# Kernel tuning notes

Hardware: AMD Instinct MI355X
Metric: run time of the kernel (lower is better)

Reference implementation:

```python
import jax, jax.numpy as jnp
import numpy as np

B, H, W, C = 64, 28, 28, 384
G = 7
N = G * G                  # tokens per window = 49
NH, HD = 12, 32            # heads, head_dim
SCALE = HD ** -0.5
EPS = 1e-5


def _make_bias_coords():
    # biases: all relative (dh, dw) offsets, shape [(2G-1)^2, 2]
    r = np.arange(1 - G, G)
    biases = np.stack(np.meshgrid(r, r, indexing='ij')).reshape(2, -1).T.astype(np.float32)
    # relative_position_index: [N, N] lookup into the bias table
    coords = np.stack(np.meshgrid(np.arange(G), np.arange(G), indexing='ij')).reshape(2, -1)
    rel = coords[:, :, None] - coords[:, None, :]          # [2, N, N]
    rel = rel.transpose(1, 2, 0)                            # [N, N, 2]
    rel[:, :, 0] += G - 1
    rel[:, :, 1] += G - 1
    rel[:, :, 0] *= 2 * G - 1
    idx = rel.sum(-1)                                       # [N, N]
    return jnp.asarray(biases), jnp.asarray(idx, dtype=jnp.int32)

BIASES, REL_IDX = _make_bias_coords()


def _ln(x, g, b):
    m = jnp.mean(x, -1, keepdims=True)
    v = jnp.var(x, -1, keepdims=True)
    return (x - m) * jax.lax.rsqrt(v + EPS) * g + b


def _pos_bias(ppw, ppb, l1g, l1b, p1w, p1b, l2g, l2b, p2w, p2b, l3g, l3b, p3w, p3b):
    # DynamicPosBias with residual=False: pos3(pos2(pos1(pos_proj(biases))))
    pos = BIASES @ ppw + ppb                                # [169, 24]
    pos = jax.nn.relu(_ln(pos, l1g, l1b)) @ p1w + p1b
    pos = jax.nn.relu(_ln(pos, l2g, l2b)) @ p2w + p2b
    pos = jax.nn.relu(_ln(pos, l3g, l3b)) @ p3w + p3b       # [169, NH]
    # gather -> [N, N, NH] -> [NH, N, N]
    return pos[REL_IDX.reshape(-1)].reshape(N, N, NH).transpose(2, 0, 1)


def _forward(x, norm1_g, norm1_b, qkv_w, qkv_b, proj_w, proj_b,
             norm2_g, norm2_b, fc1_w, fc1_b, fc2_w, fc2_b,
             pp_w, pp_b, l1_g, l1_b, p1_w, p1_b, l2_g, l2_b, p2_w, p2_b,
             l3_g, l3_b, p3_w, p3_b):
    shortcut = x
    h = _ln(x, norm1_g, norm1_b).reshape(B, H, W, C)
    # SDA (lsda_flag=0) window partition: [B, H/G, G, W/G, G, C] -> windows
    h = h.reshape(B, H // G, G, W // G, G, C).transpose(0, 1, 3, 2, 4, 5)
    h = h.reshape(-1, N, C)                                 # [B*nW, N, C]
    Bw = h.shape[0]

    qkv = (h @ qkv_w + qkv_b).reshape(Bw, N, 3, NH, HD).transpose(2, 0, 3, 1, 4)
    q, k, v = qkv[0] * SCALE, qkv[1], qkv[2]                # [Bw, NH, N, HD]

    bias = _pos_bias(pp_w, pp_b, l1_g, l1_b, p1_w, p1_b,
                     l2_g, l2_b, p2_w, p2_b, l3_g, l3_b, p3_w, p3_b)
    attn = jnp.einsum('bhnd,bhmd->bhnm', q, k) + bias[None]  # [Bw, NH, N, N]
    attn = jax.nn.softmax(attn, axis=-1)

    o = jnp.einsum('bhnm,bhmd->bhnd', attn, v)
    o = o.transpose(0, 2, 1, 3).reshape(Bw, N, C)
    o = o @ proj_w + proj_b

    # reverse window partition
    o = o.reshape(B, H // G, W // G, G, G, C).transpose(0, 1, 3, 2, 4, 5)
    o = o.reshape(B, H * W, C)

    x = shortcut + o
    y = _ln(x, norm2_g, norm2_b)
    y = jax.nn.gelu(y @ fc1_w + fc1_b, approximate=False) @ fc2_w + fc2_b
    return x + y


def setup_inputs() -> dict:
    key = jax.random.key(0)
    ks = iter(jax.random.split(key, 32))
    s = 0.02
    PD = 24  # pos_dim = (dim // 4) // 4
    MH = 4 * C

    def rn(k, shape):
        return jax.random.normal(k, shape, dtype=jnp.float32) * s

    return {
        'x': jax.random.normal(next(ks), (B, H * W, C), dtype=jnp.float32),
        'norm1_g': jnp.ones((C,), jnp.float32), 'norm1_b': jnp.zeros((C,), jnp.float32),
        'qkv_w': rn(next(ks), (C, 3 * C)), 'qkv_b': jnp.zeros((3 * C,), jnp.float32),
        'proj_w': rn(next(ks), (C, C)), 'proj_b': jnp.zeros((C,), jnp.float32),
        'norm2_g': jnp.ones((C,), jnp.float32), 'norm2_b': jnp.zeros((C,), jnp.float32),
        'fc1_w': rn(next(ks), (C, MH)), 'fc1_b': jnp.zeros((MH,), jnp.float32),
        'fc2_w': rn(next(ks), (MH, C)), 'fc2_b': jnp.zeros((C,), jnp.float32),
        'pp_w': rn(next(ks), (2, PD)), 'pp_b': jnp.zeros((PD,), jnp.float32),
        'l1_g': jnp.ones((PD,), jnp.float32), 'l1_b': jnp.zeros((PD,), jnp.float32),
        'p1_w': rn(next(ks), (PD, PD)), 'p1_b': jnp.zeros((PD,), jnp.float32),
        'l2_g': jnp.ones((PD,), jnp.float32), 'l2_b': jnp.zeros((PD,), jnp.float32),
        'p2_w': rn(next(ks), (PD, PD)), 'p2_b': jnp.zeros((PD,), jnp.float32),
        'l3_g': jnp.ones((PD,), jnp.float32), 'l3_b': jnp.zeros((PD,), jnp.float32),
        'p3_w': rn(next(ks), (PD, NH)), 'p3_b': jnp.zeros((NH,), jnp.float32),
    }


def reference(x, norm1_g, norm1_b, qkv_w, qkv_b, proj_w, proj_b,
              norm2_g, norm2_b, fc1_w, fc1_b, fc2_w, fc2_b,
              pp_w, pp_b, l1_g, l1_b, p1_w, p1_b, l2_g, l2_b, p2_w, p2_b,
              l3_g, l3_b, p3_w, p3_b):
    return _forward(x, norm1_g, norm1_b, qkv_w, qkv_b, proj_w, proj_b,
                    norm2_g, norm2_b, fc1_w, fc1_b, fc2_w, fc2_b,
                    pp_w, pp_b, l1_g, l1_b, p1_w, p1_b, l2_g, l2_b, p2_w, p2_b,
                    l3_g, l3_b, p3_w, p3_b)
```

## Files before the change

### kernel.cpp

```cpp
#include <hip/hip_runtime.h>

typedef unsigned short u16;
typedef short s16x8 __attribute__((ext_vector_type(8)));
typedef short s16x4 __attribute__((ext_vector_type(4)));
typedef float f32x4 __attribute__((ext_vector_type(4)));
typedef float f32x2 __attribute__((ext_vector_type(2)));

#define B_ 64
#define Hh 28
#define Ww 28
#define Cc 384
#define Gg 7
#define Nn 49
#define NH 12
#define HD 32
#define TT 50176
#define NWIN 1024
#define QKV_ELEMS 19267584u
#define SCALE_Q 0.17677669529663687f

__device__ __forceinline__ float b2f(u16 u) {
  union { unsigned int i; float f; } v; v.i = ((unsigned int)u) << 16; return v.f;
}
__device__ __forceinline__ u16 f2b(float f) {
  union { float f; unsigned int i; } v; v.f = f;
  unsigned int r = v.i + 0x7fffu + ((v.i >> 16) & 1u);
  return (u16)(r >> 16);
}

__device__ __forceinline__ void gload_lds16(const u16* g, u16* l) {
  __builtin_amdgcn_global_load_lds(
      (const __attribute__((address_space(1))) unsigned int*)(const void*)g,
      (__attribute__((address_space(3))) unsigned int*)(void*)l, 16, 0, 0);
}

__global__ void transpose_all(const float* __restrict__ w0, u16* __restrict__ o0,
                              const float* __restrict__ w1, u16* __restrict__ o1,
                              const float* __restrict__ w2, u16* __restrict__ o2,
                              const float* __restrict__ w3, u16* __restrict__ o3) {
  int b = blockIdx.x;
  const float* in; u16* out; int K, N, base;
  if (b < 1728)      { in = w0; out = o0; K = 384;  N = 1152; base = b; }
  else if (b < 2304) { in = w1; out = o1; K = 384;  N = 384;  base = b - 1728; }
  else if (b < 4608) { in = w2; out = o2; K = 384;  N = 1536; base = b - 2304; }
  else               { in = w3; out = o3; K = 1536; N = 384;  base = b - 4608; }
  int i = base * 256 + threadIdx.x;
  if (i < K * N) {
    int k = i / N, n = i % N;
    out[(size_t)n * K + k] = f2b(in[i]);
  }
}

__global__ __launch_bounds__(256)
void pos_mlp_kernel(const float* __restrict__ pp_w, const float* __restrict__ pp_b,
                    const float* __restrict__ l1g, const float* __restrict__ l1b,
                    const float* __restrict__ p1w, const float* __restrict__ p1b,
                    const float* __restrict__ l2g, const float* __restrict__ l2b,
                    const float* __restrict__ p2w, const float* __restrict__ p2b,
                    const float* __restrict__ l3g, const float* __restrict__ l3b,
                    const float* __restrict__ p3w, const float* __restrict__ p3b,
                    float* __restrict__ pos169) {
  __shared__ float w0[48], bb0[24], g1[24], e1[24], w1[576], bb1[24],
                   g2[24], e2[24], w2[576], bb2[24], g3[24], e3[24], w3[288], bb3[12];
  int tid = threadIdx.x;
  for (int i = tid; i < 48; i += 256) w0[i] = pp_w[i];
  for (int i = tid; i < 24; i += 256) {
    bb0[i] = pp_b[i]; g1[i] = l1g[i]; e1[i] = l1b[i]; bb1[i] = p1b[i];
    g2[i] = l2g[i]; e2[i] = l2b[i]; bb2[i] = p2b[i];
    g3[i] = l3g[i]; e3[i] = l3b[i];
  }
  for (int i = tid; i < 576; i += 256) { w1[i] = p1w[i]; w2[i] = p2w[i]; }
  for (int i = tid; i < 288; i += 256) w3[i] = p3w[i];
  for (int i = tid; i < 12; i += 256) bb3[i] = p3b[i];
  __syncthreads();
  if (tid < 169) {
    float bi = (float)(tid / 13) - 6.f, bj = (float)(tid % 13) - 6.f;
    float cur[24], t[24];
    #pragma unroll
    for (int c = 0; c < 24; c++) cur[c] = bi * w0[c] + bj * w0[24 + c] + bb0[c];

    auto lnrelu = [&](const float* gg, const float* ee) {
      float s = 0.f, sq = 0.f;
      #pragma unroll
      for (int c = 0; c < 24; c++) { s += cur[c]; sq += cur[c] * cur[c]; }
      float mean = s * (1.f / 24.f);
      float var = sq * (1.f / 24.f) - mean * mean;
      float rstd = rsqrtf(var + 1e-5f);
      #pragma unroll
      for (int c = 0; c < 24; c++)
        t[c] = fmaxf(0.f, (cur[c] - mean) * rstd * gg[c] + ee[c]);
    };

    lnrelu(g1, e1);
    #pragma unroll
    for (int o = 0; o < 24; o++) {
      float a = bb1[o];
      #pragma unroll
      for (int c = 0; c < 24; c++) a += t[c] * w1[c * 24 + o];
      cur[o] = a;
    }
    lnrelu(g2, e2);
    #pragma unroll
    for (int o = 0; o < 24; o++) {
      float a = bb2[o];
      #pragma unroll
      for (int c = 0; c < 24; c++) a += t[c] * w2[c * 24 + o];
      cur[o] = a;
    }
    lnrelu(g3, e3);
    #pragma unroll
    for (int h = 0; h < 12; h++) {
      float a = bb3[h];
      #pragma unroll
      for (int c = 0; c < 24; c++) a += t[c] * w3[c * 12 + h];
      pos169[tid * 12 + h] = a;
    }
  }
}

__global__ __launch_bounds__(256)
void ln_kernel(const float* __restrict__ x, const float* __restrict__ g,
               const float* __restrict__ be, u16* __restrict__ out) {
  int wid = threadIdx.x >> 6, lane = threadIdx.x & 63;
  size_t row = (size_t)blockIdx.x * 4 + wid;
  const float* xr = x + row * Cc;
  float v[6];
  float s = 0.f, sq = 0.f;
  #pragma unroll
  for (int p = 0; p < 3; p++) {
    f32x2 u = *(const f32x2*)&xr[p * 128 + lane * 2];
    v[2 * p] = u.x; v[2 * p + 1] = u.y;
    s += u.x + u.y; sq += u.x * u.x + u.y * u.y;
  }
  #pragma unroll
  for (int off = 32; off > 0; off >>= 1) { s += __shfl_xor(s, off); sq += __shfl_xor(sq, off); }
  float mean = s * (1.f / 384.f);
  float var = sq * (1.f / 384.f) - mean * mean;
  float rstd = rsqrtf(var + 1e-5f);
  u16* orow = out + row * Cc;
  #pragma unroll
  for (int p = 0; p < 3; p++) {
    int c = p * 128 + lane * 2;
    f32x2 ug = *(const f32x2*)&g[c];
    f32x2 ub = *(const f32x2*)&be[c];
    float o0 = (v[2 * p] - mean) * rstd * ug.x + ub.x;
    float o1 = (v[2 * p + 1] - mean) * rstd * ug.y + ub.y;
    unsigned int uo = (unsigned int)f2b(o0) | ((unsigned int)f2b(o1) << 16);
    *(unsigned int*)&orow[c] = uo;
  }
}

template <int EPI>
__global__ __launch_bounds__(256, 4)
void gemm_k(const u16* __restrict__ A, const u16* __restrict__ Bt,
            const float* __restrict__ bias, const void* resv, void* outv,
            int K, int gridX, int rowoff) {
  __shared__ u16 As[2][4096];
  __shared__ u16 Bs[2][4096];
  const int tid = threadIdx.x;
  const int wid = tid >> 6, lane = tid & 63;
  const int wr = (wid >> 1) * 64, wc = (wid & 1) * 64;
  const int lm = lane & 15, lq = lane >> 4;

  const int total = gridDim.x;
  const int xcd = blockIdx.x & 7, pos = blockIdx.x >> 3;
  const int cbase = total >> 3, crem = total & 7;
  const int tile = (xcd < crem) ? (xcd * (cbase + 1) + pos)
                                : (crem * (cbase + 1) + (xcd - crem) * cbase + pos);
  const int mTile = tile / gridX;
  const int nTile = tile - mTile * gridX;
  const int mBase = mTile * 128, nBase = nTile * 128;

  const int srow = tid >> 2;
  const int sg = (tid & 3) ^ ((tid >> 3) & 3);
  const size_t aRow0 = (size_t)(mBase + srow) * K + sg * 8;
  const size_t aRow1 = (size_t)(mBase + 64 + srow) * K + sg * 8;
  const size_t bRow0 = (size_t)(nBase + srow) * K + sg * 8;
  const size_t bRow1 = (size_t)(nBase + 64 + srow) * K + sg * 8;

  int aslot[4], bslot[4];
  #pragma unroll
  for (int i = 0; i < 4; i++) {
    int ar = wr + i * 16 + lm;
    aslot[i] = ar * 32 + (lq ^ ((ar >> 1) & 3)) * 8;
    int br = wc + i * 16 + lm;
    bslot[i] = br * 32 + (lq ^ ((br >> 1) & 3)) * 8;
  }

  auto stage = [&](int k0, int b) {
    gload_lds16(A + aRow0 + k0, As[b] + tid * 8);
    gload_lds16(A + aRow1 + k0, As[b] + 2048 + tid * 8);
    gload_lds16(Bt + bRow0 + k0, Bs[b] + tid * 8);
    gload_lds16(Bt + bRow1 + k0, Bs[b] + 2048 + tid * 8);
  };

  const int kIters = K >> 5;
  f32x4 acc[4][4] = {};
  stage(0, 0);
  __syncthreads();
  for (int k = 0; k < kIters; k++) {
    const int cb = k & 1;
    if (k + 1 < kIters) stage((k + 1) << 5, cb ^ 1);
    s16x8 af[4], bfr[4];
    #pragma unroll
    for (int i = 0; i < 4; i++) af[i] = *(const s16x8*)&As[cb][aslot[i]];
    #pragma unroll
    for (int j = 0; j < 4; j++) bfr[j] = *(const s16x8*)&Bs[cb][bslot[j]];
    #pragma unroll
    for (int i = 0; i < 4; i++)
      #pragma unroll
      for (int j = 0; j < 4; j++)
        acc[i][j] = __builtin_amdgcn_mfma_f32_16x16x32_bf16(af[i], bfr[j], acc[i][j], 0, 0, 0);
    __syncthreads();
  }

  int colA[4]; float bvv[4];
  #pragma unroll
  for (int j = 0; j < 4; j++) {
    colA[j] = nBase + wc + j * 16 + lm;
    bvv[j] = bias[colA[j]];
  }

  if constexpr (EPI == 0) {
    u16* out = (u16*)outv;
    size_t offj[4]; float scl[4];
    #pragma unroll
    for (int j = 0; j < 4; j++) {
      int col = colA[j];
      int qi = col / 384, c2 = col % 384;
      int head = c2 >> 5, d = c2 & 31;
      offj[j] = (size_t)qi * QKV_ELEMS + (size_t)head * 1568 + d;
      scl[j] = (qi == 0) ? SCALE_Q : 1.0f;
    }
    #pragma unroll
    for (int i = 0; i < 4; i++) {
      #pragma unroll
      for (int rg = 0; rg < 4; rg++) {
        int t = mBase + wr + i * 16 + lq * 4 + rg;
        int b_ = t / 784, rr = t % 784;
        int hh = rr / 28, ww = rr % 28;
        int widx = b_ * 16 + (hh / 7) * 4 + (ww / 7);
        int n = (hh % 7) * 7 + (ww % 7);
        size_t offr = (size_t)widx * 18816 + n * 32;
        #pragma unroll
        for (int j = 0; j < 4; j++)
          out[offj[j] + offr] = f2b((acc[i][j][rg] + bvv[j]) * scl[j]);
      }
    }
  } else if constexpr (EPI == 1) {
    float* out = (float*)outv;
    const float* res = (const float*)resv;
    #pragma unroll
    for (int i = 0; i < 4; i++) {
      #pragma unroll
      for (int rg = 0; rg < 4; rg++) {
        size_t rb = (size_t)(rowoff + mBase + wr + i * 16 + lq * 4 + rg) * 384;
        #pragma unroll
        for (int j = 0; j < 4; j++) {
          size_t o = rb + colA[j];
          out[o] = acc[i][j][rg] + bvv[j] + res[o];
        }
      }
    }
  } else {
    u16* out = (u16*)outv;
    #pragma unroll
    for (int i = 0; i < 4; i++) {
      #pragma unroll
      for (int rg = 0; rg < 4; rg++) {
        size_t rb = (size_t)(mBase + wr + i * 16 + lq * 4 + rg) * 1536;
        #pragma unroll
        for (int j = 0; j < 4; j++) {
          float v = acc[i][j][rg] + bvv[j];
          float gl = 0.5f * v * (1.0f + erff(v * 0.70710678118654752f));
          out[rb + colA[j]] = f2b(gl);
        }
      }
    }
  }
}

__global__ __launch_bounds__(256, 3)
void attn_mfma(const u16* __restrict__ qkv, const float* __restrict__ pos169,
               u16* __restrict__ attn_out) {
  __shared__ u16 P_l[4][64 * 68];
  __shared__ float bias_l[4][170];
  const int wid = threadIdx.x >> 6, lane = threadIdx.x & 63;
  const int lm = lane & 15, lq = lane >> 4;
  const int pair = blockIdx.x * 4 + wid;
  const int widx = pair / 12, head = pair % 12;
  const u16* qp = qkv + (size_t)widx * 18816 + head * 1568;
  const u16* kp = qp + QKV_ELEMS;
  const u16* vp = kp + QKV_ELEMS;

  for (int i = lane; i < 169; i += 64) bias_l[wid][i] = pos169[i * 12 + head];

  s16x8 aq[4], bk[4];
  #pragma unroll
  for (int i = 0; i < 4; i++) aq[i] = *(const s16x8*)&qp[(i * 16 + lm) * 32 + lq * 8];
  #pragma unroll
  for (int j = 0; j < 4; j++) bk[j] = *(const s16x8*)&kp[(j * 16 + lm) * 32 + lq * 8];

  f32x4 acc[4][4] = {};
  #pragma unroll
  for (int i = 0; i < 4; i++)
    #pragma unroll
    for (int j = 0; j < 4; j++)
      acc[i][j] = __builtin_amdgcn_mfma_f32_16x16x32_bf16(aq[i], bk[j], acc[i][j], 0, 0, 0);

  int mj[4], mhj[4], mwj[4];
  #pragma unroll
  for (int j = 0; j < 4; j++) {
    mj[j] = j * 16 + lm; mhj[j] = mj[j] / 7; mwj[j] = mj[j] - mhj[j] * 7;
  }

  #pragma unroll
  for (int i = 0; i < 4; i++) {
    #pragma unroll
    for (int rg = 0; rg < 4; rg++) {
      int n = i * 16 + lq * 4 + rg;
      int nh = n / 7, nw = n - nh * 7;
      float s[4];
      #pragma unroll
      for (int j = 0; j < 4; j++) {
        int idx = (nh - mhj[j] + 6) * 13 + (nw - mwj[j] + 6);
        idx = min(max(idx, 0), 168);
        s[j] = acc[i][j][rg] + bias_l[wid][idx];
        if (mj[j] >= 49) s[j] = -3.0e30f;
      }
      float mx = fmaxf(fmaxf(s[0], s[1]), fmaxf(s[2], s[3]));
      #pragma unroll
      for (int off = 1; off < 16; off <<= 1) mx = fmaxf(mx, __shfl_xor(mx, off));
      float e[4];
      float sm = 0.f;
      #pragma unroll
      for (int j = 0; j < 4; j++) { e[j] = __expf(s[j] - mx); sm += e[j]; }
      #pragma unroll
      for (int off = 1; off < 16; off <<= 1) sm += __shfl_xor(sm, off);
      float r = 1.0f / sm;
      #pragma unroll
      for (int j = 0; j < 4; j++)
        P_l[wid][n * 68 + mj[j]] = f2b(e[j] * r);
    }
  }

  s16x8 ap[4][2];
  #pragma unroll
  for (int i = 0; i < 4; i++)
    #pragma unroll
    for (int ks = 0; ks < 2; ks++) {
      const u16* p = &P_l[wid][(i * 16 + lm) * 68 + ks * 32 + lq * 8];
      s16x4 lo = *(const s16x4*)p;
      s16x4 hi = *(const s16x4*)(p + 4);
      ap[i][ks] = __builtin_shufflevector(lo, hi, 0, 1, 2, 3, 4, 5, 6, 7);
    }
  s16x8 bv[2][2];
  #pragma unroll
  for (int jt = 0; jt < 2; jt++)
    #pragma unroll
    for (int ks = 0; ks < 2; ks++) {
      s16x8 v;
      #pragma unroll
      for (int jj = 0; jj < 8; jj++)
        v[jj] = (short)vp[(ks * 32 + lq * 8 + jj) * 32 + jt * 16 + lm];
      bv[jt][ks] = v;
    }

  f32x4 o[4][2] = {};
  #pragma unroll
  for (int i = 0; i < 4; i++)
    #pragma unroll
    for (int jt = 0; jt < 2; jt++)
      #pragma unroll
      for (int ks = 0; ks < 2; ks++)
        o[i][jt] = __builtin_amdgcn_mfma_f32_16x16x32_bf16(ap[i][ks], bv[jt][ks], o[i][jt], 0, 0, 0);

  const int b_ = widx >> 4, wq = widx & 15;
  const int hbase = (wq >> 2) * 7, wbase = (wq & 3) * 7;
  #pragma unroll
  for (int i = 0; i < 4; i++) {
    #pragma unroll
    for (int rg = 0; rg < 4; rg++) {
      int n = i * 16 + lq * 4 + rg;
      if (n < 49) {
        int nh = n / 7, nw = n - nh * 7;
        int t = b_ * 784 + (hbase + nh) * 28 + (wbase + nw);
        size_t ob = (size_t)t * 384 + head * 32 + lm;
        attn_out[ob] = f2b(o[i][0][rg]);
        attn_out[ob + 16] = f2b(o[i][1][rg]);
      }
    }
  }
}

extern "C" void kernel_launch(void* const* d_in, const int* in_sizes, int n_in,
                              void* d_out, int out_size, void* d_ws, size_t ws_size,
                              hipStream_t stream) {
  const float* x      = (const float*)d_in[0];
  const float* n1g    = (const float*)d_in[1];
  const float* n1b    = (const float*)d_in[2];
  const float* qkv_w  = (const float*)d_in[3];
  const float* qkv_b  = (const float*)d_in[4];
  const float* proj_w = (const float*)d_in[5];
  const float* proj_b = (const float*)d_in[6];
  const float* n2g    = (const float*)d_in[7];
  const float* n2b    = (const float*)d_in[8];
  const float* fc1_w  = (const float*)d_in[9];
  const float* fc1_b  = (const float*)d_in[10];
  const float* fc2_w  = (const float*)d_in[11];
  const float* fc2_b  = (const float*)d_in[12];

  const size_t SZ_A = 115605504;
  const size_t SZ_B = 38535168;
  char* wsb = (char*)d_ws;
  u16* regA     = (u16*)wsb;
  u16* regB     = (u16*)(wsb + SZ_A);
  float* pos169 = (float*)(wsb + SZ_A + SZ_B);
  u16* qkvT     = (u16*)(wsb + SZ_A + SZ_B + 8192);
  u16* projT    = qkvT + 442368;
  u16* fc1T     = projT + 147456;
  u16* fc2T     = fc1T + 589824;

  float* out = (float*)d_out;

  transpose_all<<<6912, 256, 0, stream>>>(qkv_w, qkvT, proj_w, projT,
                                          fc1_w, fc1T, fc2_w, fc2T);

  pos_mlp_kernel<<<1, 256, 0, stream>>>(
      (const float*)d_in[13], (const float*)d_in[14], (const float*)d_in[15], (const float*)d_in[16],
      (const float*)d_in[17], (const float*)d_in[18], (const float*)d_in[19], (const float*)d_in[20],
      (const float*)d_in[21], (const float*)d_in[22], (const float*)d_in[23], (const float*)d_in[24],
      (const float*)d_in[25], (const float*)d_in[26], pos169);

  ln_kernel<<<TT / 4, 256, 0, stream>>>(x, n1g, n1b, regB);

  gemm_k<0><<<392 * 9, 256, 0, stream>>>(regB, qkvT, qkv_b, nullptr, regA,
                                         384, 9, 0);

  attn_mfma<<<NWIN * NH / 4, 256, 0, stream>>>(regA, pos169, regB);

  gemm_k<1><<<392 * 3, 256, 0, stream>>>(regB, projT, proj_b, x, out,
                                         384, 3, 0);

  ln_kernel<<<TT / 4, 256, 0, stream>>>(out, n2g, n2b, regB);

  for (int ch = 0; ch < 2; ch++) {
    const u16* h2c = regB + (size_t)ch * 25088 * 384;
    gemm_k<2><<<196 * 12, 256, 0, stream>>>(h2c, fc1T, fc1_b, nullptr, regA,
                                            384, 12, 0);
    gemm_k<1><<<196 * 3, 256, 0, stream>>>(regA, fc2T, fc2_b, out, out,
                                           1536, 3, ch * 25088);
  }
}
```

Measured before the change: 656.6 us.

## Load GEMM MFMA fragments directly from global memory, dropping LDS staging

The GEMM kernel no longer stages A and B tiles through double-buffered LDS with global_load_lds and barriers. Each wave now reads its bf16 fragments straight from global memory into registers inside a fully unrolled K loop, with K made a template parameter. Occupancy bounds drop from 4 to 2 blocks per CU. This removes LDS traffic and synchronisation, but loses the reuse of shared tiles across waves, so global and L2 traffic goes up. The fully unrolled K=1536 loop also adds register pressure.

```diff
diff --git a/kernel.cpp b/kernel.cpp
--- a/kernel.cpp
+++ b/kernel.cpp
@@ -26,12 +26,6 @@
   union { float f; unsigned int i; } v; v.f = f;
   unsigned int r = v.i + 0x7fffu + ((v.i >> 16) & 1u);
   return (u16)(r >> 16);
-}
-
-__device__ __forceinline__ void gload_lds16(const u16* g, u16* l) {
-  __builtin_amdgcn_global_load_lds(
-      (const __attribute__((address_space(1))) unsigned int*)(const void*)g,
-      (__attribute__((address_space(3))) unsigned int*)(void*)l, 16, 0, 0);
 }
 
 __global__ void transpose_all(const float* __restrict__ w0, u16* __restrict__ o0,
@@ -150,13 +144,11 @@
   }
 }
 
-template <int EPI>
-__global__ __launch_bounds__(256, 4)
+template <int EPI, int KK>
+__global__ __launch_bounds__(256, 2)
 void gemm_k(const u16* __restrict__ A, const u16* __restrict__ Bt,
             const float* __restrict__ bias, const void* resv, void* outv,
-            int K, int gridX, int rowoff) {
-  __shared__ u16 As[2][4096];
-  __shared__ u16 Bs[2][4096];
+            int gridX, int rowoff) {
   const int tid = threadIdx.x;
   const int wid = tid >> 6, lane = tid & 63;
   const int wr = (wid >> 1) * 64, wc = (wid & 1) * 64;
@@ -171,47 +163,27 @@
   const int nTile = tile - mTile * gridX;
   const int mBase = mTile * 128, nBase = nTile * 128;
 
-  const int srow = tid >> 2;
-  const int sg = (tid & 3) ^ ((tid >> 3) & 3);
-  const size_t aRow0 = (size_t)(mBase + srow) * K + sg * 8;
-  const size_t aRow1 = (size_t)(mBase + 64 + srow) * K + sg * 8;
-  const size_t bRow0 = (size_t)(nBase + srow) * K + sg * 8;
-  const size_t bRow1 = (size_t)(nBase + 64 + srow) * K + sg * 8;
-
-  int aslot[4], bslot[4];
+  const u16* ap[4];
+  const u16* bp[4];
   #pragma unroll
   for (int i = 0; i < 4; i++) {
-    int ar = wr + i * 16 + lm;
-    aslot[i] = ar * 32 + (lq ^ ((ar >> 1) & 3)) * 8;
-    int br = wc + i * 16 + lm;
-    bslot[i] = br * 32 + (lq ^ ((br >> 1) & 3)) * 8;
-  }
-
-  auto stage = [&](int k0, int b) {
-    gload_lds16(A + aRow0 + k0, As[b] + tid * 8);
-    gload_lds16(A + aRow1 + k0, As[b] + 2048 + tid * 8);
-    gload_lds16(Bt + bRow0 + k0, Bs[b] + tid * 8);
-    gload_lds16(Bt + bRow1 + k0, Bs[b] + 2048 + tid * 8);
-  };
-
-  const int kIters = K >> 5;
+    ap[i] = A + (size_t)(mBase + wr + i * 16 + lm) * KK + lq * 8;
+    bp[i] = Bt + (size_t)(nBase + wc + i * 16 + lm) * KK + lq * 8;
+  }
+
   f32x4 acc[4][4] = {};
-  stage(0, 0);
-  __syncthreads();
-  for (int k = 0; k < kIters; k++) {
-    const int cb = k & 1;
-    if (k + 1 < kIters) stage((k + 1) << 5, cb ^ 1);
+  #pragma unroll
+  for (int k0 = 0; k0 < KK; k0 += 32) {
     s16x8 af[4], bfr[4];
     #pragma unroll
-    for (int i = 0; i < 4; i++) af[i] = *(const s16x8*)&As[cb][aslot[i]];
-    #pragma unroll
-    for (int j = 0; j < 4; j++) bfr[j] = *(const s16x8*)&Bs[cb][bslot[j]];
+    for (int i = 0; i < 4; i++) af[i] = *(const s16x8*)(ap[i] + k0);
+    #pragma unroll
+    for (int j = 0; j < 4; j++) bfr[j] = *(const s16x8*)(bp[j] + k0);
     #pragma unroll
     for (int i = 0; i < 4; i++)
       #pragma unroll
       for (int j = 0; j < 4; j++)
         acc[i][j] = __builtin_amdgcn_mfma_f32_16x16x32_bf16(af[i], bfr[j], acc[i][j], 0, 0, 0);
-    __syncthreads();
   }
 
   int colA[4]; float bvv[4];
@@ -434,21 +406,17 @@
 
   ln_kernel<<<TT / 4, 256, 0, stream>>>(x, n1g, n1b, regB);
 
-  gemm_k<0><<<392 * 9, 256, 0, stream>>>(regB, qkvT, qkv_b, nullptr, regA,
-                                         384, 9, 0);
+  gemm_k<0, 384><<<392 * 9, 256, 0, stream>>>(regB, qkvT, qkv_b, nullptr, regA, 9, 0);
 
   attn_mfma<<<NWIN * NH / 4, 256, 0, stream>>>(regA, pos169, regB);
 
-  gemm_k<1><<<392 * 3, 256, 0, stream>>>(regB, projT, proj_b, x, out,
-                                         384, 3, 0);
+  gemm_k<1, 384><<<392 * 3, 256, 0, stream>>>(regB, projT, proj_b, x, out, 3, 0);
 
   ln_kernel<<<TT / 4, 256, 0, stream>>>(out, n2g, n2b, regB);
 
   for (int ch = 0; ch < 2; ch++) {
     const u16* h2c = regB + (size_t)ch * 25088 * 384;
-    gemm_k<2><<<196 * 12, 256, 0, stream>>>(h2c, fc1T, fc1_b, nullptr, regA,
-                                            384, 12, 0);
-    gemm_k<1><<<196 * 3, 256, 0, stream>>>(regA, fc2T, fc2_b, out, out,
-                                           1536, 3, ch * 25088);
-  }
-}
+    gemm_k<2, 384><<<196 * 12, 256, 0, stream>>>(h2c, fc1T, fc1_b, nullptr, regA, 12, 0);
+    gemm_k<1, 1536><<<196 * 3, 256, 0, stream>>>(regA, fc2T, fc2_b, out, out, 3, ch * 25088);
+  }
+}
```

New measurement: 1.084 ms. 1.65x slower.
